# Performance work log

Measured on AMD Instinct MI355X. Metric: run time of the kernel, lower is better.

The kernel has to match this reference:

```python
import jax, jax.numpy as jnp
import numpy as np

PCR = np.array([-75.2, -75.2, -2.0, 75.2, 75.2, 4.0], np.float32)
VSZ = np.array([0.1, 0.1, 0.15], np.float32)
RADIUS_ROI = 2.4   # sample_radius_with_roi
NUM_KP = 2048      # num_keypoints
BEV_STRIDE = 8
R_RAW = 0.8        # raw-points ball radius
R_C3 = 1.6         # x_conv3 ball radius


def _roi_valid_mask(pxyz, rois):
    # pxyz: [N,3], rois: [R,7] -> bool [N]; sample_points_with_roi math
    d = jnp.linalg.norm(pxyz[:, None, :] - rois[None, :, 0:3], axis=-1)  # [N,R]
    min_d = d.min(axis=-1)
    ridx = jnp.argmin(d, axis=-1)
    roi_max = jnp.linalg.norm(rois[ridx, 3:6] * 0.5, axis=-1)
    return min_d < roi_max + RADIUS_ROI


def _fps(xyz, valid, k):
    # farthest point sampling restricted to valid points (jit-friendly stand-in
    # for sector_fps: fixed k iterations, invalid points pinned to -inf distance)
    d0 = jnp.where(valid, 1e10, -1e10).astype(jnp.float32)
    def step(d, _):
        i = jnp.argmax(d)
        nd = jnp.sum((xyz - xyz[i]) ** 2, axis=-1)
        return jnp.minimum(d, jnp.where(valid, nd, -1e10)), i
    _, idxs = jax.lax.scan(step, d0, None, length=k)
    return idxs


def _bilinear(im, x, y):
    # im: [H,W,C]; faithful to bilinear_interpolate_torch (clamp then weight)
    H, W = im.shape[0], im.shape[1]
    x0 = jnp.clip(jnp.floor(x).astype(jnp.int32), 0, W - 1)
    x1 = jnp.clip(x0 + 1, 0, W - 1)
    y0 = jnp.clip(jnp.floor(y).astype(jnp.int32), 0, H - 1)
    y1 = jnp.clip(y0 + 1, 0, H - 1)
    Ia, Ib, Ic, Id = im[y0, x0], im[y1, x0], im[y0, x1], im[y1, x1]
    xf0, xf1 = x0.astype(x.dtype), x1.astype(x.dtype)
    yf0, yf1 = y0.astype(y.dtype), y1.astype(y.dtype)
    wa = (xf1 - x) * (yf1 - y)
    wb = (xf1 - x) * (y - yf0)
    wc = (x - xf0) * (yf1 - y)
    wd = (x - xf0) * (y - yf0)
    return Ia * wa[:, None] + Ib * wb[:, None] + Ic * wc[:, None] + Id * wd[:, None]


def _aggregate(kp, sxyz, sfeat, radius, W, b):
    # PointNet-style local aggregation: per-point MLP then radius-masked pooling
    d2 = jnp.sum((kp[:, None, :] - sxyz[None, :, :]) ** 2, axis=-1)  # [K,N]
    m = (d2 < radius * radius).astype(sfeat.dtype)
    f = jax.nn.relu(sfeat @ W + b)  # [N,C_out]
    cnt = jnp.maximum(m.sum(axis=-1, keepdims=True), 1.0)
    return (m @ f) / cnt  # [K,C_out]


def reference(points, bboxes, spatial_features, conv3_points, W_raw, b_raw, W_c3, b_c3, W_fuse, bn_gamma, bn_beta, bn_mean, bn_var):
    pxyz = points[..., 0:3]
    # 1) sectorized proposal-centric keypoint sampling (ROI filter + FPS)
    valid = jax.vmap(_roi_valid_mask)(pxyz, bboxes)
    idxs = jax.vmap(lambda x, v: _fps(x, v, NUM_KP))(pxyz, valid)  # [B,K]
    keypoints = jnp.take_along_axis(pxyz, idxs[..., None], axis=1)  # [B,K,3]
    # 2) BEV bilinear interpolation at keypoints
    xi = (keypoints[..., 0] - PCR[0]) / VSZ[0] / BEV_STRIDE
    yi = (keypoints[..., 1] - PCR[1]) / VSZ[1] / BEV_STRIDE
    bev = jnp.transpose(spatial_features, (0, 2, 3, 1))  # [B,H,W,C]
    bev_feats = jax.vmap(_bilinear)(bev, xi, yi)  # [B,K,256]
    # 3) local aggregation from raw points and x_conv3 voxel centers
    raw_agg = jax.vmap(lambda kp, s: _aggregate(kp, s[:, :3], s[:, 3:], R_RAW, W_raw, b_raw))(keypoints, points)
    c3_agg = jax.vmap(lambda kp, s: _aggregate(kp, s[:, :3], s[:, 3:], R_C3, W_c3, b_c3))(keypoints, conv3_points)
    # 4) fusion: Linear(bias=False) + BatchNorm1d (inference) + ReLU
    feats = jnp.concatenate([bev_feats, raw_agg, c3_agg], axis=-1)
    B, K, C = feats.shape
    x = feats.reshape(B * K, C) @ W_fuse
    x = (x - bn_mean) * jax.lax.rsqrt(bn_var + 1e-5) * bn_gamma + bn_beta
    return jax.nn.relu(x), keypoints


def setup_inputs() -> dict:
    key = jax.random.key(0)
    ks = jax.random.split(key, 12)
    B, N, M, R = 2, 16384, 8192, 128
    lo = jnp.array([-75.2, -75.2, -2.0], jnp.float32)
    span = jnp.array([150.4, 150.4, 6.0], jnp.float32)
    pxyz = jax.random.uniform(ks[0], (B, N, 3)) * span + lo
    pfeat = jax.random.normal(ks[1], (B, N, 2))
    points = jnp.concatenate([pxyz, pfeat], axis=-1)
    ctr = jax.random.uniform(ks[2], (B, R, 3)) * span + lo
    dims = jax.random.uniform(ks[3], (B, R, 3)) * jnp.array([3.0, 2.0, 1.0]) + jnp.array([2.0, 1.5, 1.2])
    yaw = jax.random.uniform(ks[4], (B, R, 1)) * (2.0 * np.pi)
    bboxes = jnp.concatenate([ctr, dims, yaw], axis=-1)
    spatial_features = jax.random.normal(ks[5], (B, 256, 188, 188))
    cxyz = jax.random.uniform(ks[6], (B, M, 3)) * span + lo
    cfeat = jax.random.normal(ks[7], (B, M, 64))
    conv3_points = jnp.concatenate([cxyz, cfeat], axis=-1)
    W_raw = jax.random.normal(ks[8], (2, 32)) * 0.1
    W_c3 = jax.random.normal(ks[9], (64, 64)) * 0.05
    W_fuse = jax.random.normal(ks[10], (256 + 32 + 64, 128)) * 0.05
    return dict(points=points, bboxes=bboxes, spatial_features=spatial_features,
                conv3_points=conv3_points, W_raw=W_raw, b_raw=jnp.zeros(32), W_c3=W_c3,
                b_c3=jnp.zeros(64), W_fuse=W_fuse, bn_gamma=jnp.ones(128),
                bn_beta=jnp.zeros(128), bn_mean=jnp.zeros(128), bn_var=jnp.ones(128))
```

## Files before the change

### kernel.cpp

```cpp
#include <hip/hip_runtime.h>
#include <stdint.h>

#define BN_ 2
#define NPT 16384
#define MPT 8192
#define NROI 128
#define KP 2048

typedef unsigned long long u64;
typedef unsigned u32;
typedef float v2f __attribute__((ext_vector_type(2)));

#define FEATS_LEN (4096*352)
#define CNTR_OFF  (FEATS_LEN)
#define CNTC_OFF  (CNTR_OFF + 4096)
#define FRAW_OFF  (CNTC_OFF + 4096)
#define FRAW_LEN  (BN_*NPT*32)
#define GC3_OFF   (FRAW_OFF + FRAW_LEN)
#define GC3_LEN   (BN_*MPT*64)
#define FLAGS_F_OFF (GC3_OFF + GC3_LEN)
#define PX_OFF    (FLAGS_F_OFF + (BN_*NPT)/4)
#define PY_OFF    (PX_OFF + BN_*NPT)
#define PZ_OFF    (PY_OFF + BN_*NPT)
#define OUT_KP_OFF (4096*128)

#define FPS_BLOCKS  2
#define GC3_BLOCKS  2048
#define ZERO_BLOCKS 177
#define TOTAL_BLOCKS (FPS_BLOCKS + GC3_BLOCKS + ZERO_BLOCKS)

template <int CTRL>
__device__ __forceinline__ u32 dppmov(u32 v) {
    return (u32)__builtin_amdgcn_update_dpp((int)v, (int)v, CTRL, 0xF, 0xF, false);
}
__device__ __forceinline__ u32 wave_umax32_dpp(u32 v) {
#define STG(C) { u32 o = dppmov<C>(v); v = (o > v) ? o : v; }
    STG(0x111) STG(0x112) STG(0x114) STG(0x118) STG(0x142) STG(0x143)
#undef STG
    return (u32)__builtin_amdgcn_readlane((int)v, 63);
}

__device__ __forceinline__ v2f pk_add(v2f a, v2f b) {
    v2f r; asm("v_pk_add_f32 %0, %1, %2" : "=v"(r) : "v"(a), "v"(b)); return r;
}
__device__ __forceinline__ v2f pk_mul(v2f a, v2f b) {
    v2f r; asm("v_pk_mul_f32 %0, %1, %2" : "=v"(r) : "v"(a), "v"(b)); return r;
}

__global__ void k_flags(const float* __restrict__ pts, const float* __restrict__ bbox,
                        unsigned char* __restrict__ flags,
                        const float* __restrict__ Wr, const float* __restrict__ br,
                        float* __restrict__ fraw) {
#pragma clang fp contract(off)
    __shared__ float rx[NROI], ry[NROI], rz[NROI], rt[NROI];
    __shared__ float w0[32], w1[32], bs[32];
    int b = blockIdx.x >> 6;
    int t = threadIdx.x;
    if (t < NROI) {
        const float* rr = bbox + (size_t)(b * NROI + t) * 7;
        rx[t] = rr[0]; ry[t] = rr[1]; rz[t] = rr[2];
        float hx = rr[3] * 0.5f, hy = rr[4] * 0.5f, hz = rr[5] * 0.5f;
        rt[t] = sqrtf(((hx * hx) + (hy * hy)) + (hz * hz)) + 2.4f;
    }
    if (t >= 224) { int c = t - 224; w0[c] = Wr[c]; w1[c] = Wr[32 + c]; bs[c] = br[c]; }
    __syncthreads();
    int p = (blockIdx.x & 63) * 256 + t;
    int n = b * NPT + p;
    const float* pr = pts + (size_t)n * 5;
    float x = pr[0], y = pr[1], z = pr[2];
    float mind = 3.4e38f, th = 0.f;
    for (int r = 0; r < NROI; ++r) {
        float dx = x - rx[r], dy = y - ry[r], dz = z - rz[r];
        float ds = sqrtf(((dx * dx) + (dy * dy)) + (dz * dz));
        if (ds < mind) { mind = ds; th = rt[r]; }
    }
    flags[n] = (mind < th) ? 1 : 0;
    float f3 = pr[3], f4 = pr[4];
    float* fo = fraw + (size_t)n * 32;
#pragma unroll 8
    for (int c = 0; c < 32; ++c)
        fo[c] = fmaxf(fmaf(f3, w0[c], fmaf(f4, w1[c], bs[c])), 0.f);
}

template <int NS>
__device__ __forceinline__ void fps_loop(
    int t, int lane, int w, int V,
    const float* __restrict__ pxg, const float* __restrict__ pyg,
    const float* __restrict__ pzg,
    u64 (*rkey)[8],
    float* kbuf,
    float* __restrict__ kout) {
#pragma clang fp contract(off)
    constexpr int NP = NS / 2;
    v2f px[NP], py[NP], pz[NP];
    float d[NS];
    int base = t * NS;
#pragma unroll
    for (int m = 0; m < NP; ++m) {
        int id0 = base + 2 * m;
        v2f qx = ((const v2f*)pxg)[base / 2 + m];
        v2f qy = ((const v2f*)pyg)[base / 2 + m];
        v2f qz = ((const v2f*)pzg)[base / 2 + m];
        bool in0 = id0 < V, in1 = (id0 + 1) < V;
        px[m].x = in0 ? qx.x : 1e18f;  px[m].y = in1 ? qx.y : 1e18f;
        py[m].x = in0 ? qy.x : 1e18f;  py[m].y = in1 ? qy.y : 1e18f;
        pz[m].x = in0 ? qz.x : 1e18f;  pz[m].y = in1 ? qz.y : 1e18f;
        d[2 * m]     = in0 ? 1e10f : 0.0f;
        d[2 * m + 1] = in1 ? 1e10f : 0.0f;
    }

    float bestD = -3.4e38f; int bestJ = 0;
#pragma unroll
    for (int j = 0; j < NS; ++j)
        if (d[j] > bestD) { bestD = d[j]; bestJ = j; }
    u32 gid = (u32)(base + bestJ);
    u32 ord = __float_as_uint(bestD);
    u32 maxOrd = wave_umax32_dpp(ord);
    u64 eq = __ballot(ord == maxOrd);
    int L = __builtin_ctzll(eq);
    u32 winGid = (u32)__builtin_amdgcn_readlane((int)gid, L);
    if (lane == 0) rkey[0][w] = ((u64)maxOrd << 14) | (u64)(0x3FFFu - winGid);
    __syncthreads();

    for (int k = 0; k < KP; ++k) {
        int p = k & 1;
        const u64* kq = rkey[p];
        u64 c0 = kq[0], c1 = kq[1], c2 = kq[2], c3 = kq[3];
        u64 c4 = kq[4], c5 = kq[5], c6 = kq[6], c7 = kq[7];
        u64 m0 = c0 > c1 ? c0 : c1;
        u64 m1 = c2 > c3 ? c2 : c3;
        u64 m2 = c4 > c5 ? c4 : c5;
        u64 m3 = c6 > c7 ? c6 : c7;
        u64 n0 = m0 > m1 ? m0 : m1;
        u64 n1 = m2 > m3 ? m2 : m3;
        u64 win = n0 > n1 ? n0 : n1;
        u32 wid = 0x3FFFu - ((u32)win & 0x3FFFu);
        float wx = pxg[wid], wy = pyg[wid], wz = pzg[wid];
        if (t == 0) { kbuf[k * 3] = wx; kbuf[k * 3 + 1] = wy; kbuf[k * 3 + 2] = wz; }
        v2f wnx; wnx.x = -wx; wnx.y = -wx;
        v2f wny; wny.x = -wy; wny.y = -wy;
        v2f wnz; wnz.x = -wz; wnz.y = -wz;

        bestD = -3.4e38f; bestJ = 0;
#pragma unroll
        for (int m = 0; m < NP; ++m) {
            v2f dx = pk_add(px[m], wnx);
            v2f dy = pk_add(py[m], wny);
            v2f dz = pk_add(pz[m], wnz);
            v2f s  = pk_mul(dx, dx);
            v2f s2 = pk_mul(dy, dy);
            v2f s3 = pk_mul(dz, dz);
            s = pk_add(s, s2);
            s = pk_add(s, s3);
            float dn0 = fminf(d[2 * m], s.x);
            float dn1 = fminf(d[2 * m + 1], s.y);
            d[2 * m] = dn0; d[2 * m + 1] = dn1;
            if (dn0 > bestD) { bestD = dn0; bestJ = 2 * m; }
            if (dn1 > bestD) { bestD = dn1; bestJ = 2 * m + 1; }
        }
        gid = (u32)(base + bestJ);
        ord = __float_as_uint(bestD);
        maxOrd = wave_umax32_dpp(ord);
        eq = __ballot(ord == maxOrd);
        L = __builtin_ctzll(eq);
        winGid = (u32)__builtin_amdgcn_readlane((int)gid, L);
        if (lane == 0) rkey[p ^ 1][w] = ((u64)maxOrd << 14) | (u64)(0x3FFFu - winGid);
        __syncthreads();
    }
    for (int i = t; i < KP * 3; i += 512) kout[i] = kbuf[i];
}

__global__ void __launch_bounds__(512, 2)
k_fps(const float* __restrict__ pts, const unsigned char* __restrict__ flags,
      float* __restrict__ pxw, float* __restrict__ pyw, float* __restrict__ pzw,
      float* __restrict__ kpOut,
      const float* __restrict__ conv3, const float* __restrict__ Wc,
      const float* __restrict__ bc, float* __restrict__ gc3,
      float* __restrict__ zbase) {
#pragma clang fp contract(off)
    __shared__ __align__(16) unsigned char smem[24768];
    int bid = blockIdx.x;
    int t = threadIdx.x;

    if (bid >= FPS_BLOCKS + GC3_BLOCKS) {
        float4* z4 = (float4*)zbase;
        int idx = (bid - FPS_BLOCKS - GC3_BLOCKS) * 512 + t;
        const int STRIDE = ZERO_BLOCKS * 512;
#pragma unroll
        for (int k = 0; k < 4; ++k)
            z4[idx + k * STRIDE] = make_float4(0.f, 0.f, 0.f, 0.f);
        return;
    }
    if (bid >= FPS_BLOCKS) {
        float* w = (float*)smem;
        float (*rf)[64] = (float(*)[64])(smem + 16384);
        for (int i = t; i < 4096; i += 512) w[i] = Wc[i];
        int r = (bid - FPS_BLOCKS) * 8 + (t >> 6);
        int c = t & 63;
        rf[t >> 6][c] = conv3[(size_t)r * 67 + 3 + c];
        __syncthreads();
        float s = bc[c];
#pragma unroll 8
        for (int k = 0; k < 64; ++k) s = fmaf(rf[t >> 6][k], w[k * 64 + c], s);
        gc3[(size_t)r * 64 + c] = fmaxf(s, 0.f);
        return;
    }

    u64 (*rkey)[8] = (u64(*)[8])smem;
    int* wtot      = (int*)(smem + 128);
    float* kbuf    = (float*)(smem + 160);

    int b = bid;
    int lane = t & 63, w = t >> 6;
    int chunk = t * 32;
    const float* pbase = pts + (size_t)b * NPT * 5;
    const unsigned char* fbase = flags + b * NPT;
    float* pxg = pxw + (size_t)b * NPT;
    float* pyg = pyw + (size_t)b * NPT;
    float* pzg = pzw + (size_t)b * NPT;

    int cnt = 0;
    for (int j = 0; j < 32; ++j) cnt += fbase[chunk + j] ? 1 : 0;
    int incl = cnt;
#pragma unroll
    for (int off = 1; off < 64; off <<= 1) {
        int v = __shfl_up(incl, off, 64);
        if (lane >= off) incl += v;
    }
    if (lane == 63) wtot[w] = incl;
    __syncthreads();
    int waveBase = 0, V = 0;
    for (int i = 0; i < 8; ++i) { int wv = wtot[i]; V += wv; if (i < w) waveBase += wv; }
    int pos = waveBase + incl - cnt;

    for (int j = 0; j < 32; ++j) {
        if (fbase[chunk + j]) {
            const float* pr = pbase + (size_t)(chunk + j) * 5;
            pxg[pos] = pr[0]; pyg[pos] = pr[1]; pzg[pos] = pr[2];
            ++pos;
        }
    }
    __syncthreads();

    float* kout = kpOut + (size_t)b * KP * 3;
    if (V == 0) {
        if (t == 0)
            for (int k = 0; k < KP; ++k) {
                kout[k * 3] = pbase[0]; kout[k * 3 + 1] = pbase[1]; kout[k * 3 + 2] = pbase[2];
            }
        return;
    }
    int jm = (V + 511) >> 9;
    if (jm <= 10)      fps_loop<10>(t, lane, w, V, pxg, pyg, pzg, rkey, kbuf, kout);
    else if (jm <= 12) fps_loop<12>(t, lane, w, V, pxg, pyg, pzg, rkey, kbuf, kout);
    else if (jm <= 14) fps_loop<14>(t, lane, w, V, pxg, pyg, pzg, rkey, kbuf, kout);
    else if (jm <= 16) fps_loop<16>(t, lane, w, V, pxg, pyg, pzg, rkey, kbuf, kout);
    else if (jm <= 24) fps_loop<24>(t, lane, w, V, pxg, pyg, pzg, rkey, kbuf, kout);
    else               fps_loop<32>(t, lane, w, V, pxg, pyg, pzg, rkey, kbuf, kout);
}

__global__ void k_rawagg(const float* __restrict__ pts, const float* __restrict__ kp,
                         const float* __restrict__ fraw, float* __restrict__ feats,
                         float* __restrict__ cntR) {
    __shared__ float sp[2560];
    int bid = blockIdx.x;
    int b = bid >> 7, kb = (bid >> 4) & 7, s = bid & 15;
    int t = threadIdx.x;
    int kk = kb * 256 + t, row = b * KP + kk;
    float kx = kp[row * 3], ky = kp[row * 3 + 1], kz = kp[row * 3 + 2];
    float acc[32];
#pragma unroll
    for (int c = 0; c < 32; ++c) acc[c] = 0.f;
    float cnt = 0.f;
    const float R2 = 0.8f * 0.8f;
    for (int tile = 0; tile < 2; ++tile) {
        int nbase = s * 1024 + tile * 512;
        const float* src = pts + (size_t)(b * NPT + nbase) * 5;
        for (int i = t; i < 2560; i += 256) sp[i] = src[i];
        __syncthreads();
        for (int j = 0; j < 512; ++j) {
            float dx = kx - sp[j * 5], dy = ky - sp[j * 5 + 1], dz = kz - sp[j * 5 + 2];
            float d2 = fmaf(dx, dx, fmaf(dy, dy, dz * dz));
            if (d2 < R2) {
                cnt += 1.f;
                const float* fp = fraw + (size_t)(b * NPT + nbase + j) * 32;
#pragma unroll
                for (int c = 0; c < 32; ++c) acc[c] += fp[c];
            }
        }
        __syncthreads();
    }
    float* dst = feats + (size_t)row * 352 + 256;
#pragma unroll
    for (int c = 0; c < 32; ++c) if (acc[c] != 0.f) atomicAdd(dst + c, acc[c]);
    if (cnt != 0.f) atomicAdd(cntR + row, cnt);
}

__global__ void k_c3agg(const float* __restrict__ conv3, const float* __restrict__ kp,
                        const float* __restrict__ gc3, float* __restrict__ feats,
                        float* __restrict__ cntC) {
    __shared__ float sq[256 * 3];
    int bid = blockIdx.x;
    int b = bid >> 7, kb = (bid >> 4) & 7, s = bid & 15;
    int t = threadIdx.x;
    int kk = kb * 256 + t, row = b * KP + kk;
    float kx = kp[row * 3], ky = kp[row * 3 + 1], kz = kp[row * 3 + 2];
    float acc[64];
#pragma unroll
    for (int c = 0; c < 64; ++c) acc[c] = 0.f;
    float cnt = 0.f;
    const float R2 = 1.6f * 1.6f;
    for (int tile = 0; tile < 2; ++tile) {
        int nbase = s * 512 + tile * 256;
        const float* src = conv3 + (size_t)(b * MPT + nbase + t) * 67;
        sq[t * 3] = src[0]; sq[t * 3 + 1] = src[1]; sq[t * 3 + 2] = src[2];
        __syncthreads();
        for (int j = 0; j < 256; ++j) {
            float dx = kx - sq[j * 3], dy = ky - sq[j * 3 + 1], dz = kz - sq[j * 3 + 2];
            float d2 = fmaf(dx, dx, fmaf(dy, dy, dz * dz));
            if (d2 < R2) {
                cnt += 1.f;
                const float* gp = gc3 + (size_t)(b * MPT + nbase + j) * 64;
#pragma unroll
                for (int c = 0; c < 64; ++c) acc[c] += gp[c];
            }
        }
        __syncthreads();
    }
    float* dst = feats + (size_t)row * 352 + 288;
#pragma unroll
    for (int c = 0; c < 64; ++c) if (acc[c] != 0.f) atomicAdd(dst + c, acc[c]);
    if (cnt != 0.f) atomicAdd(cntC + row, cnt);
}

__global__ void k_fuse(const float* __restrict__ feats, const float* __restrict__ cntR,
                       const float* __restrict__ cntC, const float* __restrict__ Wf,
                       const float* __restrict__ gma, const float* __restrict__ bta,
                       const float* __restrict__ mean, const float* __restrict__ var,
                       const float* __restrict__ sf, const float* __restrict__ kp,
                       float* __restrict__ out) {
    __shared__ float a[2][352];
    int r0 = blockIdx.x * 2;
    int t = threadIdx.x;
    for (int i = t; i < 704; i += 256) {
        int rr = i >= 352 ? 1 : 0;
        int k = i - rr * 352;
        int row = r0 + rr;
        float v;
        if (k < 256) {
            const float* kpr = kp + (size_t)row * 3;
            float x = kpr[0], y = kpr[1];
            float xi = ((x - (-75.2f)) / 0.1f) / 8.0f;
            float yi = ((y - (-75.2f)) / 0.1f) / 8.0f;
            int x0 = (int)floorf(xi); x0 = min(max(x0, 0), 187);
            int x1 = min(max(x0 + 1, 0), 187);
            int y0 = (int)floorf(yi); y0 = min(max(y0, 0), 187);
            int y1 = min(max(y0 + 1, 0), 187);
            float xf0 = (float)x0, xf1 = (float)x1, yf0 = (float)y0, yf1 = (float)y1;
            float wa = (xf1 - xi) * (yf1 - yi), wb = (xf1 - xi) * (yi - yf0);
            float wc = (xi - xf0) * (yf1 - yi), wd = (xi - xf0) * (yi - yf0);
            int bb = row >> 11;
            const float* plane = sf + (size_t)(bb * 256 + k) * 188 * 188;
            float Ia = plane[y0 * 188 + x0], Ib = plane[y1 * 188 + x0];
            float Ic = plane[y0 * 188 + x1], Id = plane[y1 * 188 + x1];
            v = Ia * wa + Ib * wb + Ic * wc + Id * wd;
        } else {
            v = feats[(size_t)row * 352 + k];
            float cn = (k < 288) ? cntR[row] : cntC[row];
            v = v / fmaxf(cn, 1.0f);
        }
        a[rr][k] = v;
    }
    __syncthreads();
    int r = t >> 7, c = t & 127;
    float s = 0.f;
#pragma unroll 4
    for (int k = 0; k < 352; ++k) s = fmaf(a[r][k], Wf[k * 128 + c], s);
    s = (s - mean[c]) * (1.0f / sqrtf(var[c] + 1e-5f)) * gma[c] + bta[c];
    out[(size_t)(r0 + r) * 128 + c] = fmaxf(s, 0.f);
}

extern "C" void kernel_launch(void* const* d_in, const int* in_sizes, int n_in,
                              void* d_out, int out_size, void* d_ws, size_t ws_size,
                              hipStream_t stream) {
    const float* pts   = (const float*)d_in[0];
    const float* bbox  = (const float*)d_in[1];
    const float* sf    = (const float*)d_in[2];
    const float* conv3 = (const float*)d_in[3];
    const float* Wraw  = (const float*)d_in[4];
    const float* braw  = (const float*)d_in[5];
    const float* Wc3   = (const float*)d_in[6];
    const float* bc3   = (const float*)d_in[7];
    const float* Wf    = (const float*)d_in[8];
    const float* gma   = (const float*)d_in[9];
    const float* bta   = (const float*)d_in[10];
    const float* mean  = (const float*)d_in[11];
    const float* var   = (const float*)d_in[12];

    float* wsf   = (float*)d_ws;
    float* feats = wsf;
    float* cntR  = wsf + CNTR_OFF;
    float* cntC  = wsf + CNTC_OFF;
    float* fraw  = wsf + FRAW_OFF;
    float* gc3   = wsf + GC3_OFF;
    unsigned char* flags = (unsigned char*)(wsf + FLAGS_F_OFF);
    float* pxw   = wsf + PX_OFF;
    float* pyw   = wsf + PY_OFF;
    float* pzw   = wsf + PZ_OFF;

    float* outp  = (float*)d_out;
    float* kpOut = outp + OUT_KP_OFF;

    k_flags<<<BN_ * 64, 256, 0, stream>>>(pts, bbox, flags, Wraw, braw, fraw);
    k_fps<<<TOTAL_BLOCKS, 512, 0, stream>>>(pts, flags, pxw, pyw, pzw, kpOut,
                                            conv3, Wc3, bc3, gc3, wsf);
    k_rawagg<<<BN_ * 128, 256, 0, stream>>>(pts, kpOut, fraw, feats, cntR);
    k_c3agg<<<BN_ * 128, 256, 0, stream>>>(conv3, kpOut, gc3, feats, cntC);
    k_fuse<<<2048, 256, 0, stream>>>(feats, cntR, cntC, Wf, gma, bta, mean, var,
                                     sf, kpOut, outp);
}
```

Baseline: 1.931 ms.

## Transpose BEV feature map to channel-last in spare FPS-kernel blocks for coalesced bilinear gathers

Adds extra blocks to the FPS kernel launch that transpose the spatial feature map from [C,H,W] to [H*W,C] in workspace through an LDS tile. The fuse kernel then reads the four bilinear corners with channel-contiguous, coalesced accesses instead of one strided gather per channel plane. This is done only when the workspace is large enough. The cost is a full read and write of the 2x256x188x188 map every call, about 72MB each way. That traffic may compete with the FPS blocks, which sit on the critical path.

Measured after the change: 1.909 ms. Within noise of the previous version (-1.1%).

```diff
diff --git a/kernel.cpp b/kernel.cpp
--- a/kernel.cpp
+++ b/kernel.cpp
@@ -22,12 +22,18 @@
 #define PX_OFF    (FLAGS_F_OFF + (BN_*NPT)/4)
 #define PY_OFF    (PX_OFF + BN_*NPT)
 #define PZ_OFF    (PY_OFF + BN_*NPT)
+#define SFT_OFF   (PZ_OFF + BN_*NPT)
+#define NPOS      (188*188)
+#define SFT_LEN   (BN_*NPOS*256)
 #define OUT_KP_OFF (4096*128)
 
 #define FPS_BLOCKS  2
 #define GC3_BLOCKS  2048
 #define ZERO_BLOCKS 177
-#define TOTAL_BLOCKS (FPS_BLOCKS + GC3_BLOCKS + ZERO_BLOCKS)
+#define PTILES      553
+#define SFT_BLOCKS  (BN_*4*PTILES)
+#define BASE_BLOCKS (FPS_BLOCKS + GC3_BLOCKS + ZERO_BLOCKS)
+#define TOTAL_BLOCKS (BASE_BLOCKS + SFT_BLOCKS)
 
 template <int CTRL>
 __device__ __forceinline__ u32 dppmov(u32 v) {
@@ -176,12 +182,41 @@
       float* __restrict__ kpOut,
       const float* __restrict__ conv3, const float* __restrict__ Wc,
       const float* __restrict__ bc, float* __restrict__ gc3,
-      float* __restrict__ zbase) {
+      float* __restrict__ zbase,
+      const float* __restrict__ sf, float* __restrict__ sfT) {
 #pragma clang fp contract(off)
     __shared__ __align__(16) unsigned char smem[24768];
     int bid = blockIdx.x;
     int t = threadIdx.x;
 
+    if (bid >= BASE_BLOCKS) {
+        int tb = bid - BASE_BLOCKS;
+        int pt = tb % PTILES;
+        int rem = tb / PTILES;
+        int kt = rem & 3;
+        int bb = rem >> 2;
+        int pos0 = pt * 64;
+        int k0 = kt * 64;
+        float* lds = (float*)smem;
+        int g = t >> 6, l = t & 63;
+        const float* src = sf + ((size_t)(bb * 256 + k0) * NPOS) + pos0;
+#pragma unroll
+        for (int i = 0; i < 8; ++i) {
+            int kl = g + 8 * i;
+            float v = (pos0 + l < NPOS) ? src[(size_t)kl * NPOS + l] : 0.f;
+            lds[kl * 65 + l] = v;
+        }
+        __syncthreads();
+        float* dst = sfT + (size_t)bb * NPOS * 256;
+#pragma unroll
+        for (int i = 0; i < 8; ++i) {
+            int pl = g + 8 * i;
+            int pos = pos0 + pl;
+            if (pos < NPOS)
+                dst[(size_t)pos * 256 + k0 + l] = lds[l * 65 + pl];
+        }
+        return;
+    }
     if (bid >= FPS_BLOCKS + GC3_BLOCKS) {
         float4* z4 = (float4*)zbase;
         int idx = (bid - FPS_BLOCKS - GC3_BLOCKS) * 512 + t;
@@ -337,7 +372,8 @@
                        const float* __restrict__ cntC, const float* __restrict__ Wf,
                        const float* __restrict__ gma, const float* __restrict__ bta,
                        const float* __restrict__ mean, const float* __restrict__ var,
-                       const float* __restrict__ sf, const float* __restrict__ kp,
+                       const float* __restrict__ sf, const float* __restrict__ sfT,
+                       int useT, const float* __restrict__ kp,
                        float* __restrict__ out) {
     __shared__ float a[2][352];
     int r0 = blockIdx.x * 2;
@@ -360,9 +396,18 @@
             float wa = (xf1 - xi) * (yf1 - yi), wb = (xf1 - xi) * (yi - yf0);
             float wc = (xi - xf0) * (yf1 - yi), wd = (xi - xf0) * (yi - yf0);
             int bb = row >> 11;
-            const float* plane = sf + (size_t)(bb * 256 + k) * 188 * 188;
-            float Ia = plane[y0 * 188 + x0], Ib = plane[y1 * 188 + x0];
-            float Ic = plane[y0 * 188 + x1], Id = plane[y1 * 188 + x1];
+            float Ia, Ib, Ic, Id;
+            if (useT) {
+                const float* bt = sfT + (size_t)bb * NPOS * 256 + k;
+                Ia = bt[(size_t)(y0 * 188 + x0) * 256];
+                Ib = bt[(size_t)(y1 * 188 + x0) * 256];
+                Ic = bt[(size_t)(y0 * 188 + x1) * 256];
+                Id = bt[(size_t)(y1 * 188 + x1) * 256];
+            } else {
+                const float* plane = sf + (size_t)(bb * 256 + k) * NPOS;
+                Ia = plane[y0 * 188 + x0]; Ib = plane[y1 * 188 + x0];
+                Ic = plane[y0 * 188 + x1]; Id = plane[y1 * 188 + x1];
+            }
             v = Ia * wa + Ib * wb + Ic * wc + Id * wd;
         } else {
             v = feats[(size_t)row * 352 + k];
@@ -407,15 +452,19 @@
     float* pxw   = wsf + PX_OFF;
     float* pyw   = wsf + PY_OFF;
     float* pzw   = wsf + PZ_OFF;
+    float* sfT   = wsf + SFT_OFF;
+
+    int useT = (ws_size >= (size_t)(SFT_OFF + SFT_LEN) * sizeof(float)) ? 1 : 0;
+    int nblocks = useT ? TOTAL_BLOCKS : BASE_BLOCKS;
 
     float* outp  = (float*)d_out;
     float* kpOut = outp + OUT_KP_OFF;
 
     k_flags<<<BN_ * 64, 256, 0, stream>>>(pts, bbox, flags, Wraw, braw, fraw);
-    k_fps<<<TOTAL_BLOCKS, 512, 0, stream>>>(pts, flags, pxw, pyw, pzw, kpOut,
-                                            conv3, Wc3, bc3, gc3, wsf);
+    k_fps<<<nblocks, 512, 0, stream>>>(pts, flags, pxw, pyw, pzw, kpOut,
+                                       conv3, Wc3, bc3, gc3, wsf, sf, sfT);
     k_rawagg<<<BN_ * 128, 256, 0, stream>>>(pts, kpOut, fraw, feats, cntR);
     k_c3agg<<<BN_ * 128, 256, 0, stream>>>(conv3, kpOut, gc3, feats, cntC);
     k_fuse<<<2048, 256, 0, stream>>>(feats, cntR, cntC, Wf, gma, bta, mean, var,
-                                     sf, kpOut, outp);
-}
+                                     sf, sfT, useT, kpOut, outp);
+}
```
